# Optimization experiments

Hardware: AMD Instinct MI355X
Metric: run time of the kernel (lower is better)

The kernel has to match this reference:

```python
import jax, jax.numpy as jnp
import numpy as np

# ---- static config (from module code / init_kwargs) ----
D_MODEL = 512
D_STATE = 64
D_CONV = 4
EXPAND = 2
HEADDIM = 64
D_INNER = EXPAND * D_MODEL          # 1024
NHEADS = D_INNER // HEADDIM         # 16
D_IN_PROJ = 2 * D_INNER + 2 * D_STATE + NHEADS  # 2192
CONV_DIM = D_INNER + 2 * D_STATE    # 1152
N_LAYERS = 2
VOCAB = 32768
BATCH = 2
SEQ = 512
EPS = 1e-5


def setup_inputs() -> dict:
    key = jax.random.key(0)
    ks = jax.random.split(key, 12)
    g = lambda k, shape, s=0.02: (jax.random.normal(k, shape, jnp.float32) * s)
    return {
        "input_ids": jax.random.randint(ks[0], (BATCH, SEQ), 0, VOCAB),
        "padding_mask": jnp.zeros((BATCH, SEQ), dtype=bool),  # True = pad
        "embeddings": g(ks[1], (VOCAB, D_MODEL)),
        "in_proj_w": g(ks[2], (N_LAYERS, D_IN_PROJ, D_MODEL)),
        "conv_w": g(ks[3], (N_LAYERS, CONV_DIM, D_CONV), 0.1),
        "conv_b": jnp.zeros((N_LAYERS, CONV_DIM), jnp.float32),
        "dt_bias": g(ks[4], (N_LAYERS, NHEADS), 0.5),
        "A_log": jnp.log(jax.random.uniform(ks[5], (N_LAYERS, NHEADS), jnp.float32, 1.0, 16.0)),
        "D_ssm": jnp.ones((N_LAYERS, NHEADS), jnp.float32),
        "norm_w": jnp.ones((N_LAYERS, D_INNER), jnp.float32),
        "out_proj_w": g(ks[6], (N_LAYERS, D_MODEL, D_INNER)),
        "aggr_w": g(ks[7], (D_MODEL, 2 * D_MODEL)),
        "aggr_b": jnp.zeros((D_MODEL,), jnp.float32),
        "norm_f_w": jnp.ones((D_MODEL,), jnp.float32),
        "lm_head_w": g(ks[8], (VOCAB, D_MODEL)),
        "lm_head_b": jnp.zeros((VOCAB,), jnp.float32),
    }


def rmsnorm(x, w):
    return x * jax.lax.rsqrt(jnp.mean(x * x, axis=-1, keepdims=True) + EPS) * w


def flip_sc(X, padding_mask):
    # reverse the valid (non-pad) prefix of each sequence, leave pad positions in place
    b, l, _ = X.shape
    lengths = jnp.sum(~padding_mask, axis=1)                        # (b,)
    pos = jnp.arange(l)[None, :]                                    # (1,l)
    keep = pos < lengths[:, None]
    rev = jnp.where(keep, lengths[:, None] - 1 - pos, pos)          # (b,l)
    return jnp.take_along_axis(X, rev[:, :, None], axis=1)


def causal_conv(x, w, b):
    # x: (b,l,c); depthwise causal conv with kernel size D_CONV
    xt = jnp.transpose(x, (0, 2, 1))                                # (b,c,l)
    y = jax.lax.conv_general_dilated(
        xt, w[:, None, :], window_strides=(1,), padding=[(D_CONV - 1, 0)],
        feature_group_count=w.shape[0], dimension_numbers=("NCH", "OIH", "NCH"))
    return jnp.transpose(y + b[None, :, None], (0, 2, 1))


def ssd_scan(x, dt, A, B, C):
    # x:(b,l,h,p) dt:(b,l,h) A:(h,) B,C:(b,l,n) -> y:(b,l,h,p)
    bsz = x.shape[0]
    dA = jnp.exp(dt * A)                                            # (b,l,h)
    dtx = dt[..., None] * x                                         # (b,l,h,p)
    def step(h, inp):
        dA_t, dtx_t, B_t, C_t = inp
        h = h * dA_t[:, :, None, None] + dtx_t[..., None] * B_t[:, None, None, :]
        y = jnp.einsum("bhpn,bn->bhp", h, C_t)
        return h, y
    h0 = jnp.zeros((bsz, NHEADS, HEADDIM, D_STATE), x.dtype)
    xs = (jnp.swapaxes(dA, 0, 1), jnp.swapaxes(dtx, 0, 1),
          jnp.swapaxes(B, 0, 1), jnp.swapaxes(C, 0, 1))
    _, ys = jax.lax.scan(step, h0, xs)
    return jnp.swapaxes(ys, 0, 1)


def mamba2_block(x, wi, cw, cb, dtb, alog, dss, nw, wo):
    # Mamba2 layer with residual (EncoderLayer: mamba(X) + X)
    b, l, _ = x.shape
    zxbcdt = jnp.einsum("bld,ed->ble", x, wi)                      # (b,l,D_IN_PROJ)
    z = zxbcdt[..., :D_INNER]
    xBC = zxbcdt[..., D_INNER:D_INNER + CONV_DIM]
    dt = jax.nn.softplus(zxbcdt[..., D_INNER + CONV_DIM:] + dtb)   # (b,l,h)
    xBC = jax.nn.silu(causal_conv(xBC, cw, cb))
    xs = xBC[..., :D_INNER].reshape(b, l, NHEADS, HEADDIM)
    B = xBC[..., D_INNER:D_INNER + D_STATE]
    C = xBC[..., D_INNER + D_STATE:]
    A = -jnp.exp(alog)                                             # (h,)
    y = ssd_scan(xs, dt, A, B, C) + xs * dss[None, None, :, None]
    y = y.reshape(b, l, D_INNER)
    y = rmsnorm(y * jax.nn.silu(z), nw)                            # RMSNormGated
    return jnp.einsum("ble,de->bld", y, wo) + x


def reference(input_ids, padding_mask, embeddings, in_proj_w, conv_w, conv_b,
              dt_bias, A_log, D_ssm, norm_w, out_proj_w, aggr_w, aggr_b,
              norm_f_w, lm_head_w, lm_head_b):
    X = embeddings[input_ids]                                      # (b,l,d)
    for i in range(N_LAYERS):
        X_flip = flip_sc(X, padding_mask)
        X_f = mamba2_block(X, in_proj_w[i], conv_w[i], conv_b[i], dt_bias[i],
                           A_log[i], D_ssm[i], norm_w[i], out_proj_w[i])
        X_b = mamba2_block(X_flip, in_proj_w[i], conv_w[i], conv_b[i], dt_bias[i],
                           A_log[i], D_ssm[i], norm_w[i], out_proj_w[i])
        X_b = flip_sc(X_b, padding_mask)
        # gated bidirectional fusion
        zg = jax.nn.sigmoid(jnp.concatenate([X_f, X_b], axis=-1) @ aggr_w.T + aggr_b)
        X = zg * X_f + (1.0 - zg) * X_b
    h = rmsnorm(X, norm_f_w)
    logits = h @ lm_head_w.T + lm_head_b                            # (b,l,V)
    return logits
```

## Files before the change

### kernel.cpp

```cpp
#include <hip/hip_runtime.h>

#define SEQ    512
#define DM     512
#define DI     1024
#define NH     16
#define DS     64
#define CONVD  1152
#define DPROJ  2192
#define NPADIN 2304

typedef __attribute__((ext_vector_type(8))) short bf16x8;
typedef __attribute__((ext_vector_type(4))) float floatx4;

__device__ __forceinline__ unsigned int f2bf(float f) {
  unsigned int u = __float_as_uint(f);
  u += 0x7FFFu + ((u >> 16) & 1u);
  return u >> 16;
}
__device__ __forceinline__ ushort4 cvt4(float4 v) {
  ushort4 o;
  o.x = (unsigned short)f2bf(v.x); o.y = (unsigned short)f2bf(v.y);
  o.z = (unsigned short)f2bf(v.z); o.w = (unsigned short)f2bf(v.w);
  return o;
}
__device__ __forceinline__ float sigmoidf_(float x) { return 1.f / (1.f + __expf(-x)); }
__device__ __forceinline__ float siluf_(float x) { return x * sigmoidf_(x); }

__device__ __forceinline__ void gl16(const void* g, void* l) {
  __builtin_amdgcn_global_load_lds(
      (const __attribute__((address_space(1))) unsigned int*)g,
      (__attribute__((address_space(3))) unsigned int*)l, 16, 0, 0);
}

template<int BM, int BN, int EPI>
__global__ __launch_bounds__(256) void gemm_bf(
    const short* __restrict__ A, const short* __restrict__ B,
    float* __restrict__ C, const int K, const int Nvalid, const int ldc,
    const float* __restrict__ e0, const float* __restrict__ e1,
    unsigned short* __restrict__ o2)
{
  constexpr int FM = BM / 32, FN = BN / 32;
  constexpr int CA = BM / 64, CB = BN / 64;
  __shared__ short As[BM * 32];
  __shared__ short Bs[BN * 32];
  const int tid = threadIdx.x, lane = tid & 63, wave = tid >> 6;
  const int m0 = blockIdx.y * BM, n0 = blockIdx.x * BN;
  const int wm = (wave >> 1) * (BM / 2), wn = (wave & 1) * (BN / 2);
  const int lrow = lane >> 2, lchk = (lane & 3) << 3;
  const short* agp = A + (size_t)(m0 + wave * (CA * 16) + lrow) * K + lchk;
  const short* bgp = B + (size_t)(n0 + wave * (CB * 16) + lrow) * K + lchk;
  short* albase = &As[wave * (CA * 16) * 32];
  short* blbase = &Bs[wave * (CB * 16) * 32];
  const int r16 = lane & 15, q8 = (lane >> 4) << 3;

  floatx4 acc[FM][FN];
#pragma unroll
  for (int i = 0; i < FM; i++)
#pragma unroll
    for (int j = 0; j < FN; j++) acc[i][j] = (floatx4)0.f;

  for (int k0 = 0; k0 < K; k0 += 32) {
#pragma unroll
    for (int i = 0; i < CA; ++i)
      gl16(agp + (size_t)i * 16 * K + k0, albase + i * 16 * 32);
#pragma unroll
    for (int i = 0; i < CB; ++i)
      gl16(bgp + (size_t)i * 16 * K + k0, blbase + i * 16 * 32);
    __syncthreads();
    bf16x8 afr[FM], bfr[FN];
#pragma unroll
    for (int i = 0; i < FM; i++) afr[i] = *(const bf16x8*)&As[(wm + i * 16 + r16) * 32 + q8];
#pragma unroll
    for (int j = 0; j < FN; j++) bfr[j] = *(const bf16x8*)&Bs[(wn + j * 16 + r16) * 32 + q8];
#pragma unroll
    for (int i = 0; i < FM; i++)
#pragma unroll
      for (int j = 0; j < FN; j++)
        acc[i][j] = __builtin_amdgcn_mfma_f32_16x16x32_bf16(afr[i], bfr[j], acc[i][j], 0, 0, 0);
    __syncthreads();
  }

  const int er = (lane >> 4) << 2;
#pragma unroll
  for (int i = 0; i < FM; ++i)
#pragma unroll
    for (int j = 0; j < FN; ++j)
#pragma unroll
      for (int r = 0; r < 4; ++r) {
        const int gm = m0 + wm + i * 16 + er + r;
        const int gn = n0 + wn + j * 16 + r16;
        float v = acc[i][j][r];
        if (EPI == 0) {
          if (gn < Nvalid) C[(size_t)gm * ldc + gn] = v;
        } else if (EPI == 1) {
          const int mm = gm & 1023;
          v += e0[(size_t)mm * DM + gn];
          const size_t idx = (size_t)mm * DI + ((gm >> 10) << 9) + gn;
          C[idx] = v;
          o2[idx] = (unsigned short)f2bf(v);
        } else if (EPI == 2) {
          const float zg = sigmoidf_(v + e0[gn]);
          const float xn = zg * e1[(size_t)gm * DI + gn] +
                           (1.f - zg) * e1[(size_t)gm * DI + DM + gn];
          const size_t idx = (size_t)gm * DM + gn;
          C[idx] = xn;
          o2[idx] = (unsigned short)f2bf(xn);
        } else {
          C[(size_t)gm * ldc + gn] = v + e0[gn];
        }
      }
}

#define WO4  262144
#define AW4  131072
#define LM4  4194304
__global__ void cvt3_k(const float* __restrict__ wo, const float* __restrict__ aw,
                       const float* __restrict__ lmw,
                       unsigned short* __restrict__ woB, unsigned short* __restrict__ awB,
                       unsigned short* __restrict__ lmwB) {
  const int stride = gridDim.x * blockDim.x;
  for (int i = blockIdx.x * blockDim.x + threadIdx.x; i < WO4 + AW4 + LM4; i += stride) {
    int j = i;
    const float4* s; ushort4* d;
    if (j < WO4)            { s = (const float4*)wo;  d = (ushort4*)woB; }
    else if (j < WO4 + AW4) { j -= WO4; s = (const float4*)aw;  d = (ushort4*)awB; }
    else                    { j -= WO4 + AW4; s = (const float4*)lmw; d = (ushort4*)lmwB; }
    d[j] = cvt4(s[j]);
  }
}

__global__ void cvt_wi_k(const float* __restrict__ wi, unsigned short* __restrict__ d) {
  const int row = blockIdx.x, l = blockIdx.y;
  ushort4 o; o.x = o.y = o.z = o.w = 0;
  if (row < DPROJ)
    o = cvt4(((const float4*)(wi + ((size_t)l * DPROJ + row) * DM))[threadIdx.x]);
  ((ushort4*)(d + ((size_t)l * NPADIN + row) * DM))[threadIdx.x] = o;
}

__global__ void embed_k(const int* __restrict__ ids, const float* __restrict__ emb,
                        float* __restrict__ Xf, unsigned short* __restrict__ Xb) {
  const int m = blockIdx.x;
  const int row = ids[m];
  float4 v = ((const float4*)(emb + (size_t)row * DM))[threadIdx.x];
  ((float4*)(Xf + (size_t)m * DM))[threadIdx.x] = v;
  ((ushort4*)(Xb + (size_t)m * DM))[threadIdx.x] = cvt4(v);
}

__global__ __launch_bounds__(256) void conv_k(const float* __restrict__ zx,
    const float* __restrict__ cw, const float* __restrict__ cb,
    const float* __restrict__ dtb, const float* __restrict__ alog,
    float* __restrict__ xact, float* __restrict__ dtt, float* __restrict__ dAt) {
  const int t0 = (blockIdx.x & 31) << 4;
  const int half = blockIdx.x >> 5;
  const int b = blockIdx.y;
  const float* src = zx + (size_t)b * SEQ * DPROJ + DI;
  float* d0 = xact + (size_t)b * SEQ * CONVD;
  float* d1 = xact + (size_t)(2 + b) * SEQ * CONVD;

  for (int cc = 0; cc < 3; ++cc) {
    const int ci = cc * 256 + threadIdx.x;
    if (ci >= 576) break;
    const int c = half * 576 + ci;
    const float w0 = cw[c*4+0], w1 = cw[c*4+1], w2 = cw[c*4+2], w3 = cw[c*4+3];
    const float bias = cb[c];
    float a_[22];
#pragma unroll
    for (int j = 0; j < 22; ++j) {
      const int t = t0 - 3 + j;
      a_[j] = (t >= 0 && t < SEQ) ? src[(size_t)t * DPROJ + c] : 0.f;
    }
#pragma unroll
    for (int tt = 0; tt < 16; ++tt) {
      const float f = bias + w0*a_[tt]   + w1*a_[tt+1] + w2*a_[tt+2] + w3*a_[tt+3];
      const float g = bias + w3*a_[tt+3] + w2*a_[tt+4] + w1*a_[tt+5] + w0*a_[tt+6];
      d0[(size_t)(t0+tt) * CONVD + c] = siluf_(f);
      d1[(size_t)(t0+tt) * CONVD + c] = siluf_(g);
    }
  }
  if (half == 0) {
    const int hh = threadIdx.x >> 4, tt2 = threadIdx.x & 15;
    const int t = t0 + tt2;
    const float v = zx[(size_t)(b * SEQ + t) * DPROJ + 2176 + hh] + dtb[hh];
    const float dt = (v > 15.f) ? v : log1pf(__expf(v));
    const float A = -__expf(alog[hh]);
    dtt[(b * NH + hh) * SEQ + t] = dt;
    dAt[(b * NH + hh) * SEQ + t] = __expf(dt * A);
  }
}

__global__ __launch_bounds__(256, 1) void scan_k(const float* __restrict__ xact,
    const float* __restrict__ dtt, const float* __restrict__ dAt,
    float* __restrict__ yn) {
  const int bid = blockIdx.x;
  const int dir = bid >> 7, b = (bid >> 6) & 1, h = (bid >> 2) & 15;
  const int ph = (bid >> 1) & 1, nh = bid & 1;
  const int tid = threadIdx.x, pl = tid & 31, nq = tid >> 5;
  const int p = ph * 32 + pl, nb = nq << 2;
  const float* __restrict__ src = xact + (size_t)(dir * 2 + b) * SEQ * CONVD;
  const float* __restrict__ dtp = dtt + (b * NH + h) * SEQ;
  const float* __restrict__ dap = dAt + (b * NH + h) * SEQ;
  float* __restrict__ yrow = yn + (size_t)nh * (4 * SEQ * DI)
      + (size_t)(dir * 2 + b) * SEQ * DI + h * 64 + ph * 32;
  __shared__ float yp[8][16][33];
  float hs[4] = {0.f, 0.f, 0.f, 0.f};

  for (int c0 = 0; c0 < SEQ; c0 += 16) {
#pragma unroll
    for (int s = 0; s < 16; ++s) {
      const int tn = dir ? (SEQ - 1 - (c0 + s)) : (c0 + s);
      const float* row = src + (size_t)tn * CONVD;
      const float dts = dtp[tn];
      const float das = dap[tn];
      const float xv = row[h * 64 + p];
      const float4 b4 = *(const float4*)(row + DI + nh * 32 + nb);
      const float4 c4 = *(const float4*)(row + DI + DS + nh * 32 + nb);
      const float dtx = dts * xv;
      float ya;
      hs[0] = hs[0] * das + dtx * b4.x; ya  = hs[0] * c4.x;
      hs[1] = hs[1] * das + dtx * b4.y; ya += hs[1] * c4.y;
      hs[2] = hs[2] * das + dtx * b4.z; ya += hs[2] * c4.z;
      hs[3] = hs[3] * das + dtx * b4.w; ya += hs[3] * c4.w;
      yp[nq][s][pl] = ya;
    }
    __syncthreads();
    {
      const int rt = tid >> 4, rp = (tid & 15) << 1;
      const int tn = dir ? (SEQ - 1 - (c0 + rt)) : (c0 + rt);
      float s0 = 0.f, s1 = 0.f;
#pragma unroll
      for (int j = 0; j < 8; ++j) { s0 += yp[j][rt][rp]; s1 += yp[j][rt][rp + 1]; }
      float2 o; o.x = s0; o.y = s1;
      *(float2*)&yrow[(size_t)tn * DI + rp] = o;
    }
    __syncthreads();
  }
}

__global__ __launch_bounds__(256) void p2_k(const float* __restrict__ yn,
    const float* __restrict__ xact, const float* __restrict__ zx,
    const float* __restrict__ dss, const float* __restrict__ nw,
    unsigned short* __restrict__ A2b) {
  const int m2 = blockIdx.x;
  const int e4 = threadIdx.x << 2;
  const float4 ya = *(const float4*)(yn + (size_t)m2 * DI + e4);
  const float4 yb = *(const float4*)(yn + (size_t)4 * SEQ * DI + (size_t)m2 * DI + e4);
  const float4 x4 = *(const float4*)(xact + (size_t)m2 * CONVD + e4);
  const float4 z4 = *(const float4*)(zx + (size_t)(m2 & 1023) * DPROJ + e4);
  const float d = dss[e4 >> 6];
  float4 g;
  g.x = (ya.x + yb.x + x4.x * d) * siluf_(z4.x);
  g.y = (ya.y + yb.y + x4.y * d) * siluf_(z4.y);
  g.z = (ya.z + yb.z + x4.z * d) * siluf_(z4.z);
  g.w = (ya.w + yb.w + x4.w * d) * siluf_(z4.w);
  float ss = g.x*g.x + g.y*g.y + g.z*g.z + g.w*g.w;
#pragma unroll
  for (int m = 32; m >= 1; m >>= 1) ss += __shfl_xor(ss, m);
  __shared__ float red[4];
  if ((threadIdx.x & 63) == 0) red[threadIdx.x >> 6] = ss;
  __syncthreads();
  const float tot = red[0] + red[1] + red[2] + red[3];
  const float sc = rsqrtf(tot * (1.f / 1024.f) + 1e-5f);
  const float4 w4 = *(const float4*)(nw + e4);
  float4 o;
  o.x = g.x * sc * w4.x; o.y = g.y * sc * w4.y;
  o.z = g.z * sc * w4.z; o.w = g.w * sc * w4.w;
  ((ushort4*)(A2b + (size_t)m2 * DI))[threadIdx.x] = cvt4(o);
}

__global__ __launch_bounds__(128) void fnorm_k(const float* __restrict__ X,
    const float* __restrict__ w, unsigned short* __restrict__ outb) {
  const int m = blockIdx.x;
  const int e4 = threadIdx.x << 2;
  const float4 x4 = *(const float4*)(X + (size_t)m * DM + e4);
  float ss = x4.x*x4.x + x4.y*x4.y + x4.z*x4.z + x4.w*x4.w;
#pragma unroll
  for (int mm = 32; mm >= 1; mm >>= 1) ss += __shfl_xor(ss, mm);
  __shared__ float red[2];
  if ((threadIdx.x & 63) == 0) red[threadIdx.x >> 6] = ss;
  __syncthreads();
  const float tot = red[0] + red[1];
  const float sc = rsqrtf(tot * (1.f / 512.f) + 1e-5f);
  const float4 w4 = *(const float4*)(w + e4);
  float4 o;
  o.x = x4.x * sc * w4.x; o.y = x4.y * sc * w4.y;
  o.z = x4.z * sc * w4.z; o.w = x4.w * sc * w4.w;
  ((ushort4*)(outb + (size_t)m * DM))[threadIdx.x] = cvt4(o);
}

extern "C" void kernel_launch(void* const* d_in, const int* in_sizes, int n_in,
                              void* d_out, int out_size, void* d_ws, size_t ws_size,
                              hipStream_t stream) {
  (void)in_sizes; (void)n_in; (void)out_size; (void)ws_size;
  const int*   ids  = (const int*)d_in[0];
  const float* emb  = (const float*)d_in[2];
  const float* wi   = (const float*)d_in[3];
  const float* cw   = (const float*)d_in[4];
  const float* cb   = (const float*)d_in[5];
  const float* dtb  = (const float*)d_in[6];
  const float* alog = (const float*)d_in[7];
  const float* dss  = (const float*)d_in[8];
  const float* nw   = (const float*)d_in[9];
  const float* wo   = (const float*)d_in[10];
  const float* aw   = (const float*)d_in[11];
  const float* ab   = (const float*)d_in[12];
  const float* nfw  = (const float*)d_in[13];
  const float* lmw  = (const float*)d_in[14];
  const float* lmb  = (const float*)d_in[15];
  float* out = (float*)d_out;

  float* ws    = (float*)d_ws;
  float* Xf    = ws;
  float* zx    = Xf    + (size_t)524288;
  float* xact  = zx    + (size_t)2244608;
  float* dtt   = xact  + (size_t)2359296;
  float* dAt   = dtt   + (size_t)16384;
  float* yn    = dAt   + (size_t)16384;
  float* Xcatf = yn    + (size_t)4194304;
  unsigned short* Xb    = (unsigned short*)(Xcatf + (size_t)1048576);
  unsigned short* A2b   = Xb    + (size_t)524288;
  unsigned short* Xcatb = A2b   + (size_t)2097152;
  unsigned short* hnb   = Xcatb + (size_t)1048576;
  unsigned short* wiB   = hnb   + (size_t)524288;
  unsigned short* woB   = wiB   + (size_t)2359296;
  unsigned short* awB   = woB   + (size_t)1048576;
  unsigned short* lmwB  = awB   + (size_t)524288;

  cvt_wi_k<<<dim3(NPADIN, 2), dim3(128), 0, stream>>>(wi, wiB);
  cvt3_k<<<dim3(4480), dim3(256), 0, stream>>>(wo, aw, lmw, woB, awB, lmwB);
  embed_k<<<dim3(1024), dim3(128), 0, stream>>>(ids, emb, Xf, Xb);

  for (int layer = 0; layer < 2; ++layer) {
    gemm_bf<128, 128, 0><<<dim3(18, 8), dim3(256), 0, stream>>>(
        (const short*)Xb, (const short*)(wiB + (size_t)layer * NPADIN * DM),
        zx, 512, 2192, 2192, nullptr, nullptr, nullptr);
    conv_k<<<dim3(64, 2), dim3(256), 0, stream>>>(
        zx, cw + (size_t)layer * 4608, cb + (size_t)layer * 1152,
        dtb + 16 * layer, alog + 16 * layer, xact, dtt, dAt);
    scan_k<<<dim3(256), dim3(256), 0, stream>>>(xact, dtt, dAt, yn);
    p2_k<<<dim3(2048), dim3(256), 0, stream>>>(yn, xact, zx, dss + 16 * layer,
                                               nw + (size_t)layer * 1024, A2b);
    gemm_bf<64, 128, 1><<<dim3(4, 32), dim3(256), 0, stream>>>(
        (const short*)A2b, (const short*)(woB + (size_t)layer * DM * DI),
        Xcatf, 1024, 512, 512, Xf, nullptr, Xcatb);
    gemm_bf<64, 64, 2><<<dim3(8, 16), dim3(256), 0, stream>>>(
        (const short*)Xcatb, (const short*)awB,
        Xf, 1024, 512, 512, ab, Xcatf, Xb);
  }
  fnorm_k<<<dim3(1024), dim3(128), 0, stream>>>(Xf, nfw, hnb);
  gemm_bf<128, 128, 3><<<dim3(256, 8), dim3(256), 0, stream>>>(
      (const short*)hnb, (const short*)lmwB, out, 512, 32768, 32768, lmb, nullptr, nullptr);
}
```

Before: 554.7 us.

## Use K=64 swizzled GEMM tiles, merge prep kernels, double-buffer scan reduction

The GEMM now stages 64-wide K tiles in LDS with an XOR swizzle on 16-byte chunks. That halves the number of barrier pairs per K step and is meant to avoid LDS bank conflicts on fragment reads. The three setup kernels (weight conversion and embedding) are merged into one launch to save launch overhead. The scan kernel double-buffers its partial-sum LDS array so the trailing barrier can be dropped. LDS use per block doubles in both the GEMM and the scan.

```diff
diff --git a/kernel.cpp b/kernel.cpp
--- a/kernel.cpp
+++ b/kernel.cpp
@@ -40,18 +40,19 @@
     unsigned short* __restrict__ o2)
 {
   constexpr int FM = BM / 32, FN = BN / 32;
-  constexpr int CA = BM / 64, CB = BN / 64;
-  __shared__ short As[BM * 32];
-  __shared__ short Bs[BN * 32];
+  constexpr int PA = BM / 32, PB = BN / 32;
+  __shared__ short As[BM * 64];
+  __shared__ short Bs[BN * 64];
   const int tid = threadIdx.x, lane = tid & 63, wave = tid >> 6;
   const int m0 = blockIdx.y * BM, n0 = blockIdx.x * BN;
   const int wm = (wave >> 1) * (BM / 2), wn = (wave & 1) * (BN / 2);
-  const int lrow = lane >> 2, lchk = (lane & 3) << 3;
-  const short* agp = A + (size_t)(m0 + wave * (CA * 16) + lrow) * K + lchk;
-  const short* bgp = B + (size_t)(n0 + wave * (CB * 16) + lrow) * K + lchk;
-  short* albase = &As[wave * (CA * 16) * 32];
-  short* blbase = &Bs[wave * (CB * 16) * 32];
-  const int r16 = lane & 15, q8 = (lane >> 4) << 3;
+  const int prow = wave * 8 + (lane >> 3);
+  const int schk = ((lane & 7) ^ (prow & 7)) << 3;
+  const short* agp = A + (size_t)(m0 + prow) * K + schk;
+  const short* bgp = B + (size_t)(n0 + prow) * K + schk;
+  short* albase = &As[wave * 8 * 64];
+  short* blbase = &Bs[wave * 8 * 64];
+  const int r16 = lane & 15, quad = lane >> 4;
 
   floatx4 acc[FM][FN];
 #pragma unroll
@@ -59,28 +60,37 @@
 #pragma unroll
     for (int j = 0; j < FN; j++) acc[i][j] = (floatx4)0.f;
 
-  for (int k0 = 0; k0 < K; k0 += 32) {
-#pragma unroll
-    for (int i = 0; i < CA; ++i)
-      gl16(agp + (size_t)i * 16 * K + k0, albase + i * 16 * 32);
-#pragma unroll
-    for (int i = 0; i < CB; ++i)
-      gl16(bgp + (size_t)i * 16 * K + k0, blbase + i * 16 * 32);
+  for (int k0 = 0; k0 < K; k0 += 64) {
+#pragma unroll
+    for (int p = 0; p < PA; ++p)
+      gl16(agp + (size_t)p * 32 * K + k0, albase + p * 32 * 64);
+#pragma unroll
+    for (int p = 0; p < PB; ++p)
+      gl16(bgp + (size_t)p * 32 * K + k0, blbase + p * 32 * 64);
     __syncthreads();
-    bf16x8 afr[FM], bfr[FN];
-#pragma unroll
-    for (int i = 0; i < FM; i++) afr[i] = *(const bf16x8*)&As[(wm + i * 16 + r16) * 32 + q8];
-#pragma unroll
-    for (int j = 0; j < FN; j++) bfr[j] = *(const bf16x8*)&Bs[(wn + j * 16 + r16) * 32 + q8];
-#pragma unroll
-    for (int i = 0; i < FM; i++)
-#pragma unroll
-      for (int j = 0; j < FN; j++)
-        acc[i][j] = __builtin_amdgcn_mfma_f32_16x16x32_bf16(afr[i], bfr[j], acc[i][j], 0, 0, 0);
+#pragma unroll
+    for (int kk = 0; kk < 2; ++kk) {
+      bf16x8 afr[FM], bfr[FN];
+#pragma unroll
+      for (int i = 0; i < FM; i++) {
+        const int row = wm + i * 16 + r16;
+        afr[i] = *(const bf16x8*)&As[row * 64 + (((kk * 4 + quad) ^ (row & 7)) << 3)];
+      }
+#pragma unroll
+      for (int j = 0; j < FN; j++) {
+        const int row = wn + j * 16 + r16;
+        bfr[j] = *(const bf16x8*)&Bs[row * 64 + (((kk * 4 + quad) ^ (row & 7)) << 3)];
+      }
+#pragma unroll
+      for (int i = 0; i < FM; i++)
+#pragma unroll
+        for (int j = 0; j < FN; j++)
+          acc[i][j] = __builtin_amdgcn_mfma_f32_16x16x32_bf16(afr[i], bfr[j], acc[i][j], 0, 0, 0);
+    }
     __syncthreads();
   }
 
-  const int er = (lane >> 4) << 2;
+  const int er = quad << 2;
 #pragma unroll
   for (int i = 0; i < FM; ++i)
 #pragma unroll
@@ -114,36 +124,38 @@
 #define WO4  262144
 #define AW4  131072
 #define LM4  4194304
-__global__ void cvt3_k(const float* __restrict__ wo, const float* __restrict__ aw,
-                       const float* __restrict__ lmw,
-                       unsigned short* __restrict__ woB, unsigned short* __restrict__ awB,
-                       unsigned short* __restrict__ lmwB) {
-  const int stride = gridDim.x * blockDim.x;
-  for (int i = blockIdx.x * blockDim.x + threadIdx.x; i < WO4 + AW4 + LM4; i += stride) {
-    int j = i;
-    const float4* s; ushort4* d;
-    if (j < WO4)            { s = (const float4*)wo;  d = (ushort4*)woB; }
-    else if (j < WO4 + AW4) { j -= WO4; s = (const float4*)aw;  d = (ushort4*)awB; }
-    else                    { j -= WO4 + AW4; s = (const float4*)lmw; d = (ushort4*)lmwB; }
-    d[j] = cvt4(s[j]);
-  }
-}
-
-__global__ void cvt_wi_k(const float* __restrict__ wi, unsigned short* __restrict__ d) {
-  const int row = blockIdx.x, l = blockIdx.y;
-  ushort4 o; o.x = o.y = o.z = o.w = 0;
-  if (row < DPROJ)
-    o = cvt4(((const float4*)(wi + ((size_t)l * DPROJ + row) * DM))[threadIdx.x]);
-  ((ushort4*)(d + ((size_t)l * NPADIN + row) * DM))[threadIdx.x] = o;
-}
-
-__global__ void embed_k(const int* __restrict__ ids, const float* __restrict__ emb,
-                        float* __restrict__ Xf, unsigned short* __restrict__ Xb) {
-  const int m = blockIdx.x;
-  const int row = ids[m];
-  float4 v = ((const float4*)(emb + (size_t)row * DM))[threadIdx.x];
-  ((float4*)(Xf + (size_t)m * DM))[threadIdx.x] = v;
-  ((ushort4*)(Xb + (size_t)m * DM))[threadIdx.x] = cvt4(v);
+__global__ __launch_bounds__(256) void prep_k(
+    const int* __restrict__ ids, const float* __restrict__ emb,
+    const float* __restrict__ wi, const float* __restrict__ wo,
+    const float* __restrict__ aw, const float* __restrict__ lmw,
+    float* __restrict__ Xf, unsigned short* __restrict__ Xb,
+    unsigned short* __restrict__ wiB, unsigned short* __restrict__ woB,
+    unsigned short* __restrict__ awB, unsigned short* __restrict__ lmwB) {
+  const int blk = blockIdx.x, tid = threadIdx.x;
+  if (blk < 512) {
+    const int m = blk * 2 + (tid >> 7), col = tid & 127;
+    const int row = ids[m];
+    float4 v = ((const float4*)(emb + (size_t)row * DM))[col];
+    ((float4*)(Xf + (size_t)m * DM))[col] = v;
+    ((ushort4*)(Xb + (size_t)m * DM))[col] = cvt4(v);
+  } else if (blk < 512 + 2304) {
+    const int slot = (blk - 512) * 2 + (tid >> 7), col = tid & 127;
+    const int l = slot >= 2304 ? 1 : 0;
+    const int row = slot - l * 2304;
+    ushort4 o; o.x = o.y = o.z = o.w = 0;
+    if (row < DPROJ)
+      o = cvt4(((const float4*)(wi + ((size_t)l * DPROJ + row) * DM))[col]);
+    ((ushort4*)(wiB + ((size_t)l * NPADIN + row) * DM))[col] = o;
+  } else {
+    for (int i = (blk - 2816) * 256 + tid; i < WO4 + AW4 + LM4; i += 4480 * 256) {
+      int j = i;
+      const float4* s; ushort4* d;
+      if (j < WO4)            { s = (const float4*)wo;  d = (ushort4*)woB; }
+      else if (j < WO4 + AW4) { j -= WO4; s = (const float4*)aw;  d = (ushort4*)awB; }
+      else                    { j -= WO4 + AW4; s = (const float4*)lmw; d = (ushort4*)lmwB; }
+      d[j] = cvt4(s[j]);
+    }
+  }
 }
 
 __global__ __launch_bounds__(256) void conv_k(const float* __restrict__ zx,
@@ -201,10 +213,11 @@
   const float* __restrict__ dap = dAt + (b * NH + h) * SEQ;
   float* __restrict__ yrow = yn + (size_t)nh * (4 * SEQ * DI)
       + (size_t)(dir * 2 + b) * SEQ * DI + h * 64 + ph * 32;
-  __shared__ float yp[8][16][33];
+  __shared__ float yp[2][8][16][33];
   float hs[4] = {0.f, 0.f, 0.f, 0.f};
-
-  for (int c0 = 0; c0 < SEQ; c0 += 16) {
+  int pb = 0;
+
+  for (int c0 = 0; c0 < SEQ; c0 += 16, pb ^= 1) {
 #pragma unroll
     for (int s = 0; s < 16; ++s) {
       const int tn = dir ? (SEQ - 1 - (c0 + s)) : (c0 + s);
@@ -220,7 +233,7 @@
       hs[1] = hs[1] * das + dtx * b4.y; ya += hs[1] * c4.y;
       hs[2] = hs[2] * das + dtx * b4.z; ya += hs[2] * c4.z;
       hs[3] = hs[3] * das + dtx * b4.w; ya += hs[3] * c4.w;
-      yp[nq][s][pl] = ya;
+      yp[pb][nq][s][pl] = ya;
     }
     __syncthreads();
     {
@@ -228,11 +241,10 @@
       const int tn = dir ? (SEQ - 1 - (c0 + rt)) : (c0 + rt);
       float s0 = 0.f, s1 = 0.f;
 #pragma unroll
-      for (int j = 0; j < 8; ++j) { s0 += yp[j][rt][rp]; s1 += yp[j][rt][rp + 1]; }
+      for (int j = 0; j < 8; ++j) { s0 += yp[pb][j][rt][rp]; s1 += yp[pb][j][rt][rp + 1]; }
       float2 o; o.x = s0; o.y = s1;
       *(float2*)&yrow[(size_t)tn * DI + rp] = o;
     }
-    __syncthreads();
   }
 }
 
@@ -325,9 +337,8 @@
   unsigned short* awB   = woB   + (size_t)1048576;
   unsigned short* lmwB  = awB   + (size_t)524288;
 
-  cvt_wi_k<<<dim3(NPADIN, 2), dim3(128), 0, stream>>>(wi, wiB);
-  cvt3_k<<<dim3(4480), dim3(256), 0, stream>>>(wo, aw, lmw, woB, awB, lmwB);
-  embed_k<<<dim3(1024), dim3(128), 0, stream>>>(ids, emb, Xf, Xb);
+  prep_k<<<dim3(7296), dim3(256), 0, stream>>>(ids, emb, wi, wo, aw, lmw,
+                                               Xf, Xb, wiB, woB, awB, lmwB);
 
   for (int layer = 0; layer < 2; ++layer) {
     gemm_bf<128, 128, 0><<<dim3(18, 8), dim3(256), 0, stream>>>(
```

Measured after the change: 514.2 us. -7.3%, faster.
